# Kernel optimization log

Hardware: AMD Instinct MI355X
Metric: run time of the kernel (lower is better)

Reference implementation:

```python
import jax, jax.numpy as jnp
import numpy as np

B, MAX_H, MAX_W, D, S, HID = 64, 64, 32, 512, 8, 64


def setup_inputs() -> dict:
    key = jax.random.key(0)
    ks = jax.random.split(key, 7)
    return {
        "canonical": jax.random.normal(ks[0], (S, S, D), jnp.float32) * 0.02,
        "w1": jax.random.normal(ks[1], (2, HID), jnp.float32) * 0.5,
        "b1": jax.random.normal(ks[2], (HID,), jnp.float32) * 0.1,
        "w2": jax.random.normal(ks[3], (HID, D), jnp.float32) * 0.05,
        "b2": jax.random.normal(ks[4], (D,), jnp.float32) * 0.05,
        "batch_size": B,
        "target_h_list": jax.random.randint(ks[5], (B,), 1, MAX_H + 1, jnp.int32),
        "target_w_list": jax.random.randint(ks[6], (B,), 1, MAX_W + 1, jnp.int32),
        "max_h": MAX_H,
        "max_w": MAX_W,
    }


def _axis_coords(sizes, max_len):
    # sizes: [B] clamped lengths; returns normalized coords u in [0,1] at each
    # padded position (torch.linspace(0,1,L) semantics; 0 when L==1). [B, max_len]
    idx = jnp.arange(max_len, dtype=jnp.float32)[None, :]
    L = sizes[:, None].astype(jnp.float32)
    return jnp.where(L > 1, idx / jnp.maximum(L - 1.0, 1.0), 0.0)


def _forward(canonical, w1, b1, w2, b2, target_h_list, target_w_list, max_h, max_w):
    S_ = canonical.shape[0]
    Hs = jnp.clip(target_h_list, 1, max_h)  # [B]
    Ws = jnp.clip(target_w_list, 1, max_w)  # [B]

    u = _axis_coords(Hs, max_h)  # [B, mh]
    v = _axis_coords(Ws, max_w)  # [B, mw]

    # Bilinear resize of canonical grid with align_corners=True:
    # source coord = normalized coord * (S-1)
    sy = jnp.clip(u * (S_ - 1), 0.0, S_ - 1.0)  # [B, mh]
    sx = jnp.clip(v * (S_ - 1), 0.0, S_ - 1.0)  # [B, mw]
    y0 = jnp.floor(sy).astype(jnp.int32)
    x0 = jnp.floor(sx).astype(jnp.int32)
    y1 = jnp.minimum(y0 + 1, S_ - 1)
    x1 = jnp.minimum(x0 + 1, S_ - 1)
    wy = (sy - y0.astype(jnp.float32))[:, :, None, None]  # [B, mh, 1, 1]
    wx = (sx - x0.astype(jnp.float32))[:, None, :, None]  # [B, 1, mw, 1]

    yi0 = y0[:, :, None]  # [B, mh, 1]
    yi1 = y1[:, :, None]
    xi0 = x0[:, None, :]  # [B, 1, mw]
    xi1 = x1[:, None, :]
    q00 = canonical[yi0, xi0]  # [B, mh, mw, D]
    q01 = canonical[yi0, xi1]
    q10 = canonical[yi1, xi0]
    q11 = canonical[yi1, xi1]
    bil = ((1.0 - wy) * ((1.0 - wx) * q00 + wx * q01)
           + wy * ((1.0 - wx) * q10 + wx * q11))  # [B, mh, mw, D]

    # Coordinate refinement MLP on (u, v)
    coords = jnp.stack(
        [jnp.broadcast_to(u[:, :, None], (u.shape[0], max_h, max_w)),
         jnp.broadcast_to(v[:, None, :], (u.shape[0], max_h, max_w))],
        axis=-1)  # [B, mh, mw, 2]
    h = jax.nn.gelu(coords @ w1 + b1, approximate=False)
    delta = h @ w2 + b2  # [B, mh, mw, D]

    mask = ((jnp.arange(max_h)[None, :, None] < Hs[:, None, None])
            & (jnp.arange(max_w)[None, None, :] < Ws[:, None, None]))  # [B, mh, mw]
    queries = jnp.where(mask[..., None], bil + delta, 0.0)
    return queries, mask


def reference(canonical, w1, b1, w2, b2, batch_size, target_h_list,
              target_w_list, max_h, max_w):
    return _forward(canonical, w1, b1, w2, b2, target_h_list, target_w_list,
                    max_h, max_w)
```

## Files before the change

kernel.cpp:

```cpp
#include <hip/hip_runtime.h>
#include <math.h>

#define NB    64
#define MAXH  64
#define MAXW  32
#define DCH   512
#define SS    8
#define HID   64

#define QTOTAL ((size_t)NB * MAXH * MAXW * DCH)

typedef float f4  __attribute__((ext_vector_type(4)));
typedef short s8v __attribute__((ext_vector_type(8)));

__device__ __forceinline__ float gelu_exact(float x) {
    return 0.5f * x * (1.0f + erff(x * 0.70710678118654752440f));
}

__device__ __forceinline__ unsigned short bf16_rne(float x) {
    unsigned int u = __float_as_uint(x);
    unsigned int r = u + 0x7fffu + ((u >> 16) & 1u);
    return (unsigned short)(r >> 16);
}

__global__ __launch_bounds__(256) void w2prep_kernel(
    const float* __restrict__ w2, s8v* __restrict__ w2b)
{
    const int tid  = blockIdx.x * 256 + threadIdx.x;
    const int lane = tid & 63;
    const int ct   = (tid >> 6) & 31;
    const int kh   = tid >> 11;
    const int q    = lane >> 4;
    const int m    = lane & 15;
    const int c    = ct * 16 + m;
    union { s8v v; unsigned short us[8]; } pk;
    #pragma unroll
    for (int j = 0; j < 8; ++j) {
        const int k = kh * 32 + q * 8 + j;
        pk.us[j] = bf16_rne(w2[k * DCH + c]);
    }
    w2b[tid] = pk.v;
}

__global__ __launch_bounds__(256) void hgqg_kernel(
    const float* __restrict__ canonical,
    const float* __restrict__ w1,
    const float* __restrict__ b1,
    const s8v*   __restrict__ w2b,
    const float* __restrict__ b2,
    const int*   __restrict__ hlist,
    const int*   __restrict__ wlist,
    float* __restrict__ out)
{
    const int raw  = blockIdx.x;
    const int id   = (raw ^ (raw >> 7)) & 8191;
    const int i    = id & 63;
    const int half = (id >> 6) & 1;
    const int b    = id >> 7;
    const int blk  = (b << 6) | i;
    const int t    = threadIdx.x;

    int H = hlist[b]; H = min(max(H, 1), MAXH);
    int W = wlist[b]; W = min(max(W, 1), MAXW);

    const int jbase = half << 4;

    f4* q4 = (f4*)(out + (size_t)blk * (MAXW * DCH)) + jbase * 128;

    if (half == 0 && t < MAXW) {
        out[QTOTAL + (size_t)blk * MAXW + t] = (i < H && t < W) ? 1.0f : 0.0f;
    }

    const f4 z = {0.f, 0.f, 0.f, 0.f};

    if (i >= H || jbase >= W) {
        #pragma unroll
        for (int r = 0; r < 8; ++r) q4[t + r * 256] = z;
        return;
    }

    const float u    = (H > 1) ? (float)i / (float)(H - 1) : 0.0f;
    const float sy   = fminf(u * 7.0f, 7.0f);
    const int   y0   = (int)sy;
    const int   y1   = min(y0 + 1, SS - 1);
    const float wy   = sy - (float)y0;
    const float winv = (W > 1) ? 1.0f / (float)(W - 1) : 0.0f;

    __shared__ __align__(16) float ri[SS * 516];
    {
        const f4* can4 = (const f4*)canonical;
        #pragma unroll
        for (int rr = 0; rr < 4; ++rr) {
            const int idx = t + rr * 256;
            const int x   = idx >> 7;
            const int c4  = idx & 127;
            const f4 a = can4[(y0 * SS + x) * 128 + c4];
            const f4 d = can4[(y1 * SS + x) * 128 + c4];
            *(f4*)&ri[x * 516 + c4 * 4] = a + wy * (d - a);
        }
    }

    __shared__ __align__(16) float hsh[16][68];
    {
        const int jl = t >> 4;
        const int k0 = (t & 15) * 4;
        const float v = (float)(jbase + jl) * winv;
        #pragma unroll
        for (int kk = 0; kk < 4; ++kk) {
            const int k = k0 + kk;
            hsh[jl][k] = gelu_exact(u * w1[k] + v * w1[HID + k] + b1[k]);
        }
    }
    __syncthreads();

    const int l = t & 63;
    const int w = t >> 6;
    const int q = l >> 4;
    const int m = l & 15;

    union { s8v v; unsigned short us[8]; } A0, A1;
    {
        const float* hrow = &hsh[m][q * 8];
        #pragma unroll
        for (int j = 0; j < 8; ++j) {
            A0.us[j] = bf16_rne(hrow[j]);
            A1.us[j] = bf16_rne(hrow[32 + j]);
        }
    }

    const int   jl  = jbase + m;
    const float vv  = (float)jl * winv;
    const float sx  = fminf(vv * 7.0f, 7.0f);
    const int   x0  = (int)sx;
    const int   x1  = min(x0 + 1, SS - 1);
    const float wx  = sx - (float)x0;
    const bool  jok = (jl < W);

    float* orow = out + (size_t)blk * (MAXW * DCH) + (size_t)jl * DCH;

    #pragma unroll
    for (int tt = 0; tt < 8; ++tt) {
        const int ct = w * 8 + tt;
        const int cb = ct * 16 + q * 4;

        const f4 f0 = *(const f4*)&ri[x0 * 516 + cb];
        const f4 f1 = *(const f4*)&ri[x1 * 516 + cb];
        const f4 bb = *(const f4*)&b2[cb];
        f4 acc = f0 + wx * (f1 - f0) + bb;

        const s8v b0  = w2b[ct * 64 + l];
        const s8v b1f = w2b[2048 + ct * 64 + l];
        acc = __builtin_amdgcn_mfma_f32_16x16x32_bf16(b0,  A0.v, acc, 0, 0, 0);
        acc = __builtin_amdgcn_mfma_f32_16x16x32_bf16(b1f, A1.v, acc, 0, 0, 0);

        const f4 res = jok ? acc : z;
        *(f4*)(orow + cb) = res;
    }
}

extern "C" void kernel_launch(void* const* d_in, const int* in_sizes, int n_in,
                              void* d_out, int out_size, void* d_ws, size_t ws_size,
                              hipStream_t stream) {
    const float* canonical = (const float*)d_in[0];
    const float* w1        = (const float*)d_in[1];
    const float* b1        = (const float*)d_in[2];
    const float* w2        = (const float*)d_in[3];
    const float* b2        = (const float*)d_in[4];
    const int*   hlist     = (const int*)d_in[6];
    const int*   wlist     = (const int*)d_in[7];
    float* out = (float*)d_out;
    s8v*   w2b = (s8v*)d_ws;

    w2prep_kernel<<<16, 256, 0, stream>>>(w2, w2b);
    hgqg_kernel<<<2 * NB * MAXH, 256, 0, stream>>>(
        canonical, w1, b1, w2b, b2, hlist, wlist, out);
}
```

Before: 279.8 us.

## Merge column halves into one block per row and reuse staged data

```diff
diff --git a/kernel.cpp b/kernel.cpp
--- a/kernel.cpp
+++ b/kernel.cpp
@@ -42,7 +42,7 @@
     w2b[tid] = pk.v;
 }
 
-__global__ __launch_bounds__(256) void hgqg_kernel(
+__global__ __launch_bounds__(256, 4) void hgqg_kernel(
     const float* __restrict__ canonical,
     const float* __restrict__ w1,
     const float* __restrict__ b1,
@@ -52,32 +52,30 @@
     const int*   __restrict__ wlist,
     float* __restrict__ out)
 {
-    const int raw  = blockIdx.x;
-    const int id   = (raw ^ (raw >> 7)) & 8191;
-    const int i    = id & 63;
-    const int half = (id >> 6) & 1;
-    const int b    = id >> 7;
-    const int blk  = (b << 6) | i;
-    const int t    = threadIdx.x;
+    const int raw = blockIdx.x;
+    const int b   = raw & 63;
+    const int i   = ((raw >> 6) + b) & 63;
+    const int blk = (b << 6) | i;
+    const int t   = threadIdx.x;
 
     int H = hlist[b]; H = min(max(H, 1), MAXH);
     int W = wlist[b]; W = min(max(W, 1), MAXW);
 
-    const int jbase = half << 4;
-
-    f4* q4 = (f4*)(out + (size_t)blk * (MAXW * DCH)) + jbase * 128;
-
-    if (half == 0 && t < MAXW) {
+    if (t < MAXW) {
         out[QTOTAL + (size_t)blk * MAXW + t] = (i < H && t < W) ? 1.0f : 0.0f;
     }
 
+    float* obase = out + (size_t)blk * (MAXW * DCH);
+    f4* q4 = (f4*)obase;
     const f4 z = {0.f, 0.f, 0.f, 0.f};
 
-    if (i >= H || jbase >= W) {
+    if (i >= H) {
         #pragma unroll
-        for (int r = 0; r < 8; ++r) q4[t + r * 256] = z;
+        for (int r = 0; r < 16; ++r) q4[t + r * 256] = z;
         return;
     }
+
+    const bool half1 = (W > 16);
 
     const float u    = (H > 1) ? (float)i / (float)(H - 1) : 0.0f;
     const float sy   = fminf(u * 7.0f, 7.0f);
@@ -100,15 +98,17 @@
         }
     }
 
-    __shared__ __align__(16) float hsh[16][68];
+    __shared__ __align__(16) float hsh[32][68];
     {
-        const int jl = t >> 4;
-        const int k0 = (t & 15) * 4;
-        const float v = (float)(jbase + jl) * winv;
-        #pragma unroll
-        for (int kk = 0; kk < 4; ++kk) {
-            const int k = k0 + kk;
-            hsh[jl][k] = gelu_exact(u * w1[k] + v * w1[HID + k] + b1[k]);
+        const int jl = t >> 3;
+        const int k0 = (t & 7) * 8;
+        if (jl < 16 || half1) {
+            const float v = (float)jl * winv;
+            #pragma unroll
+            for (int kk = 0; kk < 8; ++kk) {
+                const int k = k0 + kk;
+                hsh[jl][k] = gelu_exact(u * w1[k] + v * w1[HID + k] + b1[k]);
+            }
         }
     }
     __syncthreads();
@@ -118,43 +118,68 @@
     const int q = l >> 4;
     const int m = l & 15;
 
-    union { s8v v; unsigned short us[8]; } A0, A1;
+    union { s8v v; unsigned short us[8]; } A0h0, A1h0, A0h1, A1h1;
     {
-        const float* hrow = &hsh[m][q * 8];
+        const float* hrow0 = &hsh[m][q * 8];
         #pragma unroll
         for (int j = 0; j < 8; ++j) {
-            A0.us[j] = bf16_rne(hrow[j]);
-            A1.us[j] = bf16_rne(hrow[32 + j]);
-        }
-    }
-
-    const int   jl  = jbase + m;
-    const float vv  = (float)jl * winv;
-    const float sx  = fminf(vv * 7.0f, 7.0f);
-    const int   x0  = (int)sx;
-    const int   x1  = min(x0 + 1, SS - 1);
-    const float wx  = sx - (float)x0;
-    const bool  jok = (jl < W);
-
-    float* orow = out + (size_t)blk * (MAXW * DCH) + (size_t)jl * DCH;
+            A0h0.us[j] = bf16_rne(hrow0[j]);
+            A1h0.us[j] = bf16_rne(hrow0[32 + j]);
+        }
+        if (half1) {
+            const float* hrow1 = &hsh[16 + m][q * 8];
+            #pragma unroll
+            for (int j = 0; j < 8; ++j) {
+                A0h1.us[j] = bf16_rne(hrow1[j]);
+                A1h1.us[j] = bf16_rne(hrow1[32 + j]);
+            }
+        }
+    }
+
+    const float v0  = (float)m * winv;
+    const float sx0 = fminf(v0 * 7.0f, 7.0f);
+    const int   x00 = (int)sx0;
+    const int   x01 = min(x00 + 1, SS - 1);
+    const float wx0 = sx0 - (float)x00;
+    const bool  jok0 = (m < W);
+
+    const float v1  = (float)(16 + m) * winv;
+    const float sx1 = fminf(v1 * 7.0f, 7.0f);
+    const int   x10 = (int)sx1;
+    const int   x11 = min(x10 + 1, SS - 1);
+    const float wx1 = sx1 - (float)x10;
+    const bool  jok1 = (16 + m < W);
+
+    float* orow0 = obase + (size_t)m * DCH;
+    float* orow1 = obase + (size_t)(16 + m) * DCH;
 
     #pragma unroll
     for (int tt = 0; tt < 8; ++tt) {
         const int ct = w * 8 + tt;
         const int cb = ct * 16 + q * 4;
 
-        const f4 f0 = *(const f4*)&ri[x0 * 516 + cb];
-        const f4 f1 = *(const f4*)&ri[x1 * 516 + cb];
-        const f4 bb = *(const f4*)&b2[cb];
-        f4 acc = f0 + wx * (f1 - f0) + bb;
-
         const s8v b0  = w2b[ct * 64 + l];
         const s8v b1f = w2b[2048 + ct * 64 + l];
-        acc = __builtin_amdgcn_mfma_f32_16x16x32_bf16(b0,  A0.v, acc, 0, 0, 0);
-        acc = __builtin_amdgcn_mfma_f32_16x16x32_bf16(b1f, A1.v, acc, 0, 0, 0);
-
-        const f4 res = jok ? acc : z;
-        *(f4*)(orow + cb) = res;
+        const f4  bb  = *(const f4*)&b2[cb];
+
+        {
+            const f4 f0 = *(const f4*)&ri[x00 * 516 + cb];
+            const f4 f1 = *(const f4*)&ri[x01 * 516 + cb];
+            f4 acc = f0 + wx0 * (f1 - f0) + bb;
+            acc = __builtin_amdgcn_mfma_f32_16x16x32_bf16(b0,  A0h0.v, acc, 0, 0, 0);
+            acc = __builtin_amdgcn_mfma_f32_16x16x32_bf16(b1f, A1h0.v, acc, 0, 0, 0);
+            *(f4*)(orow0 + cb) = jok0 ? acc : z;
+        }
+        if (half1) {
+            const f4 g0 = *(const f4*)&ri[x10 * 516 + cb];
+            const f4 g1 = *(const f4*)&ri[x11 * 516 + cb];
+            f4 a2 = g0 + wx1 * (g1 - g0) + bb;
+            a2 = __builtin_amdgcn_mfma_f32_16x16x32_bf16(b0,  A0h1.v, a2, 0, 0, 0);
+            a2 = __builtin_amdgcn_mfma_f32_16x16x32_bf16(b1f, A1h1.v, a2, 0, 0, 0);
+            *(f4*)(orow1 + cb) = jok1 ? a2 : z;
+        } else {
+            *(f4*)(orow1 + cb) = z;
+        }
     }
 }
 
@@ -172,6 +197,6 @@
     s8v*   w2b = (s8v*)d_ws;
 
     w2prep_kernel<<<16, 256, 0, stream>>>(w2, w2b);
-    hgqg_kernel<<<2 * NB * MAXH, 256, 0, stream>>>(
+    hgqg_kernel<<<NB * MAXH, 256, 0, stream>>>(
         canonical, w1, b1, w2b, b2, hlist, wlist, out);
 }
```

After: 287.2 us. 2.7% more time.
